# Kernel optimization log

Measured on AMD Instinct MI355X. Metric: run time of the kernel, lower is better.

The kernel has to match this reference:

```python
import jax, jax.numpy as jnp
import numpy as np

B, S, D, O, R, E = 4, 2048, 4096, 4096, 16, 8
SCALING = 32.0 / 16.0  # lora_alpha / lora_rank


def setup_inputs() -> dict:
    key = jax.random.key(0)
    ks = jax.random.split(key, 7)
    x = jax.random.normal(ks[0], (B, S, D), dtype=jnp.float32)
    W_base = jax.random.normal(ks[1], (O, D), dtype=jnp.float32) * 0.02
    b_base = jnp.zeros((O,), dtype=jnp.float32)
    A_w = jax.random.normal(ks[2], (R, D), dtype=jnp.float32) * 0.02     # lora_A weight
    B_w = jax.random.normal(ks[3], (O, R), dtype=jnp.float32) * 0.02     # lora_B weight
    router_w = jax.random.normal(ks[4], (E, D), dtype=jnp.float32) * 0.02  # router weight (core_router=False -> acts on x)
    cores = jax.random.normal(ks[5], (E, R, R), dtype=jnp.float32)       # expert rank x rank cores
    return {"x": x, "W_base": W_base, "b_base": b_base, "A_w": A_w,
            "B_w": B_w, "router_w": router_w, "cores": cores}


def reference(x, W_base, b_base, A_w, B_w, router_w, cores):
    # base linear: [B,S,O]
    result = jnp.einsum('bsd,od->bso', x, W_base) + b_base
    # lora down-projection (dropout=0 -> identity): [B,S,R]
    ax = jnp.einsum('bsd,rd->bsr', x, A_w)
    # router on x (core_router=False): softmax over experts -> [B,S,E]
    probs = jax.nn.softmax(jnp.einsum('bsd,ed->bse', x, router_w), axis=-1)
    # per-token weighted core applied to ax WITHOUT materializing [B,S,R,R]:
    # first ax through each expert core [B,S,E,R], then weight-reduce over experts.
    per_expert = jnp.einsum('bsr,erq->bseq', ax, cores)
    mixed = jnp.einsum('bseq,bse->bsq', per_expert, probs)  # [B,S,R]
    result = result + jnp.einsum('bsr,or->bso', mixed, B_w) * SCALING
    return result
```

## Files before the change

### kernel.cpp

```cpp
#include <hip/hip_runtime.h>
#include <stdint.h>

#define D_DIM 4096
#define O_DIM 4096
#define M_DIM 8192
#define SCALE_F 2.0f
#define BK 32
#define NKT 128

typedef __attribute__((ext_vector_type(4))) float f32x4;
typedef __attribute__((ext_vector_type(8))) __bf16 bf16x8;
typedef __attribute__((ext_vector_type(8))) unsigned short u16x8;

__device__ __forceinline__ unsigned short f32_to_bf16_bits(float f) {
    union { float f; uint32_t u; } v; v.f = f;
    return (unsigned short)((v.u + 0x7FFFu + ((v.u >> 16) & 1u)) >> 16);
}

__device__ __forceinline__ float dot4(f32x4 a, f32x4 b) {
    return fmaf(a.x, b.x, fmaf(a.y, b.y, fmaf(a.z, b.z, a.w * b.w)));
}

__device__ __forceinline__ int swz(int b) { return b ^ (((b >> 7) & 7) << 4); }

__global__ __launch_bounds__(256) void convert_bf16_kernel(const float* __restrict__ src,
                                                           unsigned short* __restrict__ dst,
                                                           int n4) {
    int stride = gridDim.x * blockDim.x;
    for (int i = blockIdx.x * blockDim.x + threadIdx.x; i < n4; i += stride) {
        f32x4 v = ((const f32x4*)src)[i];
        ushort4 o;
        o.x = f32_to_bf16_bits(v.x);
        o.y = f32_to_bf16_bits(v.y);
        o.z = f32_to_bf16_bits(v.z);
        o.w = f32_to_bf16_bits(v.w);
        ((ushort4*)dst)[i] = o;
    }
}

__global__ __launch_bounds__(256) void partial_mixed_kernel(const float* __restrict__ x,
                                                            const float* __restrict__ A_w,
                                                            const float* __restrict__ router_w,
                                                            unsigned short* __restrict__ xbf,
                                                            float* __restrict__ ypart) {
    __shared__ __align__(16) float Xc[32][132];
    __shared__ __align__(16) float Wc[24][132];

    const int tid = threadIdx.x;
    const int t0 = blockIdx.x * 32;
    const int d0 = blockIdx.y * 512;

    const int tg = tid >> 3;
    const int og = tid & 7;
    float acc0 = 0.f, acc1 = 0.f, acc2 = 0.f;

    for (int sub = 0; sub < 4; ++sub) {
        const int dbase = d0 + sub * 128;
        __syncthreads();
        #pragma unroll
        for (int i = 0; i < 4; ++i) {
            int idx = i * 256 + tid;
            int t = idx >> 5, dq = idx & 31;
            f32x4 v = *(const f32x4*)&x[(size_t)(t0 + t) * D_DIM + dbase + dq * 4];
            *(f32x4*)&Xc[t][dq * 4] = v;
            ushort4 o;
            o.x = f32_to_bf16_bits(v.x);
            o.y = f32_to_bf16_bits(v.y);
            o.z = f32_to_bf16_bits(v.z);
            o.w = f32_to_bf16_bits(v.w);
            *(ushort4*)&xbf[(size_t)(t0 + t) * D_DIM + dbase + dq * 4] = o;
        }
        #pragma unroll
        for (int i = 0; i < 3; ++i) {
            int idx = i * 256 + tid;
            int r = idx >> 5, dq = idx & 31;
            const float* src = (r < 16) ? (A_w + (size_t)r * D_DIM)
                                        : (router_w + (size_t)(r - 16) * D_DIM);
            *(f32x4*)&Wc[r][dq * 4] = *(const f32x4*)&src[dbase + dq * 4];
        }
        __syncthreads();
        #pragma unroll
        for (int dq = 0; dq < 32; ++dq) {
            f32x4 xv = *(const f32x4*)&Xc[tg][dq * 4];
            acc0 += dot4(xv, *(const f32x4*)&Wc[og * 3 + 0][dq * 4]);
            acc1 += dot4(xv, *(const f32x4*)&Wc[og * 3 + 1][dq * 4]);
            acc2 += dot4(xv, *(const f32x4*)&Wc[og * 3 + 2][dq * 4]);
        }
    }
    float* dst = ypart + (((size_t)blockIdx.y * 256 + blockIdx.x) * 32 + tg) * 24 + og * 3;
    dst[0] = acc0; dst[1] = acc1; dst[2] = acc2;
}

__global__ __launch_bounds__(128) void finalize_mixed_kernel(const float* __restrict__ ypart,
                                                             const float* __restrict__ cores,
                                                             float* __restrict__ mixbuf) {
    __shared__ __align__(16) float Cs[2048];
    const int tid = threadIdx.x;
    #pragma unroll
    for (int i = 0; i < 4; ++i) {
        int idx = i * 128 + tid;
        ((f32x4*)Cs)[idx] = ((const f32x4*)cores)[idx];
    }
    __syncthreads();

    const int tok = blockIdx.x * 128 + tid;
    const int tile = tok >> 5, t = tok & 31;

    float y[24];
    #pragma unroll
    for (int j = 0; j < 24; ++j) y[j] = 0.f;
    for (int ds = 0; ds < 8; ++ds) {
        const float* src = ypart + (((size_t)ds * 256 + tile) * 32 + t) * 24;
        #pragma unroll
        for (int j = 0; j < 24; ++j) y[j] += src[j];
    }

    float mx = y[16];
    #pragma unroll
    for (int e = 1; e < 8; ++e) mx = fmaxf(mx, y[16 + e]);
    float p[8], psum = 0.f;
    #pragma unroll
    for (int e = 0; e < 8; ++e) { p[e] = __expf(y[16 + e] - mx); psum += p[e]; }
    const float inv = 1.0f / psum;

    float outq[16];
    #pragma unroll
    for (int q = 0; q < 16; ++q) outq[q] = 0.f;
    for (int e = 0; e < 8; ++e) {
        const float pe = p[e] * inv;
        #pragma unroll
        for (int r = 0; r < 16; ++r) {
            const float ar = y[r] * pe;
            #pragma unroll
            for (int q = 0; q < 16; ++q)
                outq[q] = fmaf(ar, Cs[(e * 16 + r) * 16 + q], outq[q]);
        }
    }
    #pragma unroll
    for (int q = 0; q < 4; ++q) {
        f32x4 v = {outq[q * 4 + 0], outq[q * 4 + 1], outq[q * 4 + 2], outq[q * 4 + 3]};
        *(f32x4*)&mixbuf[(size_t)tok * 16 + q * 4] = v;
    }
}

__global__ __launch_bounds__(512, 2) void gemm_kernel(const unsigned short* __restrict__ xbf,
                                                      const unsigned short* __restrict__ wbf,
                                                      const float* __restrict__ bias,
                                                      const float* __restrict__ Bw,
                                                      const float* __restrict__ mixbuf,
                                                      float* __restrict__ out) {
    __shared__ __align__(16) unsigned short lds[4][2][256 * 32];

    const int bid = blockIdx.x;
    const int xcd = bid & 7;
    const int lid = bid >> 3;
    const int tm = (lid >> 4) * 8 + xcd;
    const int tn = lid & 15;
    const int m0 = tm * 256, n0 = tn * 256;

    const int tid = threadIdx.x;
    const int wave = tid >> 6, lane = tid & 63;
    const int wr = wave >> 2, wcn = wave & 3;

    int aoff[2], boff[2];
    #pragma unroll
    for (int u = 0; u < 2; ++u) {
        int c = u * 512 + tid;
        int g = swz(c * 16);
        int grow = g >> 6, gc8 = (g >> 4) & 3;
        aoff[u] = (m0 + grow) * D_DIM + gc8 * 8;
        boff[u] = (n0 + grow) * D_DIM + gc8 * 8;
    }

    const int tA = lane & 15, kq = lane >> 4;
    int aRd[8], bRd[4];
    #pragma unroll
    for (int mi = 0; mi < 8; ++mi)
        aRd[mi] = swz((wr * 128 + mi * 16 + tA) * 64 + kq * 16);
    #pragma unroll
    for (int ni = 0; ni < 4; ++ni)
        bRd[ni] = swz((wcn * 64 + ni * 16 + tA) * 64 + kq * 16);

    f32x4 acc[8][4];
    const f32x4 fz = {0.f, 0.f, 0.f, 0.f};
    #pragma unroll
    for (int mi = 0; mi < 8; ++mi)
        #pragma unroll
        for (int ni = 0; ni < 4; ++ni) acc[mi][ni] = fz;

#define STAGE_UNIT(sb, kt, u, isA)                                                        \
    do {                                                                                  \
        const unsigned short* gsrc =                                                      \
            (isA) ? (xbf + aoff[u] + (kt)*BK) : (wbf + boff[u] + (kt)*BK);                \
        __builtin_amdgcn_global_load_lds(                                                 \
            (const __attribute__((address_space(1))) void*)gsrc,                          \
            (__attribute__((address_space(3))) void*)(&lds[sb][(isA) ? 0 : 1]             \
                                                         [((u)*512 + wave * 64) * 8]),    \
            16, 0, 0);                                                                    \
    } while (0)

#define K_ITER(BUF, SBUF, KT, STG, VMC)                                                   \
    {                                                                                     \
        const char* Ab = (const char*)&lds[BUF][0][0];                                    \
        const char* Bb = (const char*)&lds[BUF][1][0];                                    \
        bf16x8 b0 = __builtin_bit_cast(bf16x8, *(const u16x8*)(Bb + bRd[0]));             \
        bf16x8 b1 = __builtin_bit_cast(bf16x8, *(const u16x8*)(Bb + bRd[1]));             \
        bf16x8 b2 = __builtin_bit_cast(bf16x8, *(const u16x8*)(Bb + bRd[2]));             \
        bf16x8 b3 = __builtin_bit_cast(bf16x8, *(const u16x8*)(Bb + bRd[3]));             \
        bf16x8 a0 = __builtin_bit_cast(bf16x8, *(const u16x8*)(Ab + aRd[0]));             \
        bf16x8 a1 = __builtin_bit_cast(bf16x8, *(const u16x8*)(Ab + aRd[1]));             \
        bf16x8 a2 = __builtin_bit_cast(bf16x8, *(const u16x8*)(Ab + aRd[2]));             \
        bf16x8 a3 = __builtin_bit_cast(bf16x8, *(const u16x8*)(Ab + aRd[3]));             \
        if (STG) {                                                                        \
            STAGE_UNIT(SBUF, KT, 0, 1);                                                   \
            STAGE_UNIT(SBUF, KT, 1, 1);                                                   \
        }                                                                                 \
        asm volatile("" ::: "memory");                                                    \
        __builtin_amdgcn_s_barrier();                                                     \
        asm volatile("" ::: "memory");                                                    \
        __builtin_amdgcn_s_setprio(1);                                                    \
        acc[0][0] = __builtin_amdgcn_mfma_f32_16x16x32_bf16(a0, b0, acc[0][0], 0, 0, 0);  \
        acc[0][1] = __builtin_amdgcn_mfma_f32_16x16x32_bf16(a0, b1, acc[0][1], 0, 0, 0);  \
        acc[0][2] = __builtin_amdgcn_mfma_f32_16x16x32_bf16(a0, b2, acc[0][2], 0, 0, 0);  \
        acc[0][3] = __builtin_amdgcn_mfma_f32_16x16x32_bf16(a0, b3, acc[0][3], 0, 0, 0);  \
        acc[1][0] = __builtin_amdgcn_mfma_f32_16x16x32_bf16(a1, b0, acc[1][0], 0, 0, 0);  \
        acc[1][1] = __builtin_amdgcn_mfma_f32_16x16x32_bf16(a1, b1, acc[1][1], 0, 0, 0);  \
        acc[1][2] = __builtin_amdgcn_mfma_f32_16x16x32_bf16(a1, b2, acc[1][2], 0, 0, 0);  \
        acc[1][3] = __builtin_amdgcn_mfma_f32_16x16x32_bf16(a1, b3, acc[1][3], 0, 0, 0);  \
        acc[2][0] = __builtin_amdgcn_mfma_f32_16x16x32_bf16(a2, b0, acc[2][0], 0, 0, 0);  \
        acc[2][1] = __builtin_amdgcn_mfma_f32_16x16x32_bf16(a2, b1, acc[2][1], 0, 0, 0);  \
        acc[2][2] = __builtin_amdgcn_mfma_f32_16x16x32_bf16(a2, b2, acc[2][2], 0, 0, 0);  \
        acc[2][3] = __builtin_amdgcn_mfma_f32_16x16x32_bf16(a2, b3, acc[2][3], 0, 0, 0);  \
        acc[3][0] = __builtin_amdgcn_mfma_f32_16x16x32_bf16(a3, b0, acc[3][0], 0, 0, 0);  \
        acc[3][1] = __builtin_amdgcn_mfma_f32_16x16x32_bf16(a3, b1, acc[3][1], 0, 0, 0);  \
        acc[3][2] = __builtin_amdgcn_mfma_f32_16x16x32_bf16(a3, b2, acc[3][2], 0, 0, 0);  \
        acc[3][3] = __builtin_amdgcn_mfma_f32_16x16x32_bf16(a3, b3, acc[3][3], 0, 0, 0);  \
        __builtin_amdgcn_s_setprio(0);                                                    \
        asm volatile("" ::: "memory");                                                    \
        __builtin_amdgcn_s_barrier();                                                     \
        asm volatile("" ::: "memory");                                                    \
        bf16x8 a4 = __builtin_bit_cast(bf16x8, *(const u16x8*)(Ab + aRd[4]));             \
        bf16x8 a5 = __builtin_bit_cast(bf16x8, *(const u16x8*)(Ab + aRd[5]));             \
        bf16x8 a6 = __builtin_bit_cast(bf16x8, *(const u16x8*)(Ab + aRd[6]));             \
        bf16x8 a7 = __builtin_bit_cast(bf16x8, *(const u16x8*)(Ab + aRd[7]));             \
        if (STG) {                                                                        \
            STAGE_UNIT(SBUF, KT, 0, 0);                                                   \
            STAGE_UNIT(SBUF, KT, 1, 0);                                                   \
        }                                                                                 \
        asm volatile("s_waitcnt vmcnt(" #VMC ")" ::: "memory");                           \
        __builtin_amdgcn_s_barrier();                                                     \
        asm volatile("" ::: "memory");                                                    \
        __builtin_amdgcn_s_setprio(1);                                                    \
        acc[4][0] = __builtin_amdgcn_mfma_f32_16x16x32_bf16(a4, b0, acc[4][0], 0, 0, 0);  \
        acc[4][1] = __builtin_amdgcn_mfma_f32_16x16x32_bf16(a4, b1, acc[4][1], 0, 0, 0);  \
        acc[4][2] = __builtin_amdgcn_mfma_f32_16x16x32_bf16(a4, b2, acc[4][2], 0, 0, 0);  \
        acc[4][3] = __builtin_amdgcn_mfma_f32_16x16x32_bf16(a4, b3, acc[4][3], 0, 0, 0);  \
        acc[5][0] = __builtin_amdgcn_mfma_f32_16x16x32_bf16(a5, b0, acc[5][0], 0, 0, 0);  \
        acc[5][1] = __builtin_amdgcn_mfma_f32_16x16x32_bf16(a5, b1, acc[5][1], 0, 0, 0);  \
        acc[5][2] = __builtin_amdgcn_mfma_f32_16x16x32_bf16(a5, b2, acc[5][2], 0, 0, 0);  \
        acc[5][3] = __builtin_amdgcn_mfma_f32_16x16x32_bf16(a5, b3, acc[5][3], 0, 0, 0);  \
        acc[6][0] = __builtin_amdgcn_mfma_f32_16x16x32_bf16(a6, b0, acc[6][0], 0, 0, 0);  \
        acc[6][1] = __builtin_amdgcn_mfma_f32_16x16x32_bf16(a6, b1, acc[6][1], 0, 0, 0);  \
        acc[6][2] = __builtin_amdgcn_mfma_f32_16x16x32_bf16(a6, b2, acc[6][2], 0, 0, 0);  \
        acc[6][3] = __builtin_amdgcn_mfma_f32_16x16x32_bf16(a6, b3, acc[6][3], 0, 0, 0);  \
        acc[7][0] = __builtin_amdgcn_mfma_f32_16x16x32_bf16(a7, b0, acc[7][0], 0, 0, 0);  \
        acc[7][1] = __builtin_amdgcn_mfma_f32_16x16x32_bf16(a7, b1, acc[7][1], 0, 0, 0);  \
        acc[7][2] = __builtin_amdgcn_mfma_f32_16x16x32_bf16(a7, b2, acc[7][2], 0, 0, 0);  \
        acc[7][3] = __builtin_amdgcn_mfma_f32_16x16x32_bf16(a7, b3, acc[7][3], 0, 0, 0);  \
        __builtin_amdgcn_s_setprio(0);                                                    \
        asm volatile("s_waitcnt lgkmcnt(0)" ::: "memory");                                \
        __builtin_amdgcn_s_barrier();                                                     \
        asm volatile("" ::: "memory");                                                    \
    }

    #pragma unroll
    for (int kt = 0; kt < 3; ++kt) {
        STAGE_UNIT(kt, kt, 0, 1);
        STAGE_UNIT(kt, kt, 1, 1);
        STAGE_UNIT(kt, kt, 0, 0);
        STAGE_UNIT(kt, kt, 1, 0);
    }
    asm volatile("s_waitcnt vmcnt(8)" ::: "memory");
    __builtin_amdgcn_s_barrier();
    asm volatile("" ::: "memory");

    for (int jj = 0; jj < 31; ++jj) {
        #pragma unroll
        for (int i = 0; i < 4; ++i) {
            const int j = jj * 4 + i;
            const int kt = j + 3;
            K_ITER(i, (i + 3) & 3, kt, 1, 8);
        }
    }
    K_ITER(0, 3, 127, 1, 8);
    K_ITER(1, 0, 0, 0, 4);
    K_ITER(2, 0, 0, 0, 0);
    K_ITER(3, 0, 0, 0, 0);
#undef K_ITER
#undef STAGE_UNIT

    const int colq = lane & 15, rq = lane >> 4;
    f32x4 bwv[4][4];
    float bcol[4];
    #pragma unroll
    for (int ni = 0; ni < 4; ++ni) {
        const int col = n0 + wcn * 64 + ni * 16 + colq;
        bcol[ni] = bias[col];
        #pragma unroll
        for (int k = 0; k < 4; ++k) bwv[ni][k] = *(const f32x4*)&Bw[(size_t)col * 16 + k * 4];
    }
    #pragma unroll
    for (int mi = 0; mi < 8; ++mi) {
        #pragma unroll
        for (int j = 0; j < 4; ++j) {
            const int row = m0 + wr * 128 + mi * 16 + rq * 4 + j;
            const f32x4* mx = (const f32x4*)&mixbuf[(size_t)row * 16];
            const f32x4 m0v = mx[0], m1v = mx[1], m2v = mx[2], m3v = mx[3];
            #pragma unroll
            for (int ni = 0; ni < 4; ++ni) {
                const int col = n0 + wcn * 64 + ni * 16 + colq;
                const float lora = dot4(m0v, bwv[ni][0]) + dot4(m1v, bwv[ni][1]) +
                                   dot4(m2v, bwv[ni][2]) + dot4(m3v, bwv[ni][3]);
                out[(size_t)row * O_DIM + col] = acc[mi][ni][j] + bcol[ni] + SCALE_F * lora;
            }
        }
    }
}

extern "C" void kernel_launch(void* const* d_in, const int* in_sizes, int n_in,
                              void* d_out, int out_size, void* d_ws, size_t ws_size,
                              hipStream_t stream) {
    const float* x        = (const float*)d_in[0];
    const float* W_base   = (const float*)d_in[1];
    const float* b_base   = (const float*)d_in[2];
    const float* A_w      = (const float*)d_in[3];
    const float* B_w      = (const float*)d_in[4];
    const float* router_w = (const float*)d_in[5];
    const float* cores    = (const float*)d_in[6];
    float* out = (float*)d_out;

    char* ws = (char*)d_ws;
    unsigned short* xbf = (unsigned short*)ws;
    unsigned short* wbf = (unsigned short*)(ws + (size_t)M_DIM * D_DIM * 2);
    char* after_w = ws + (size_t)M_DIM * D_DIM * 2 + (size_t)O_DIM * D_DIM * 2;
    float* mixbuf = (float*)after_w;
    float* ypart  = (float*)(after_w + (size_t)M_DIM * 16 * 4);

    convert_bf16_kernel<<<2048, 256, 0, stream>>>(W_base, wbf, (O_DIM * D_DIM) / 4);
    partial_mixed_kernel<<<dim3(256, 8), 256, 0, stream>>>(x, A_w, router_w, xbf, ypart);
    finalize_mixed_kernel<<<64, 128, 0, stream>>>(ypart, cores, mixbuf);
    gemm_kernel<<<512, 512, 0, stream>>>(xbf, wbf, b_base, B_w, mixbuf, out);
}
```

Measured before the change: 337.8 us.

## Fold LoRA up-projection into GEMM as extra MFMA K-step; prefetch partial loads

The scaled mixed LoRA vector and B_w are stored as bf16, zero-padded to K=32, and run through one extra MFMA K-iteration in the main GEMM. This replaces the per-output scalar dot-product epilogue, which read fp32 mixbuf and Bw for every element. The LoRA path now runs in bf16 instead of fp32, which slightly reduces its precision. The partial_mixed kernel also register-prefetches the next x and weight chunk to overlap global loads with compute, and a small kernel converts B_w to bf16.

```diff
diff --git a/kernel.cpp b/kernel.cpp
--- a/kernel.cpp
+++ b/kernel.cpp
@@ -4,7 +4,6 @@
 #define D_DIM 4096
 #define O_DIM 4096
 #define M_DIM 8192
-#define SCALE_F 2.0f
 #define BK 32
 #define NKT 128
 
@@ -38,6 +37,25 @@
     }
 }
 
+__global__ __launch_bounds__(256) void bwbf_kernel(const float* __restrict__ Bw,
+                                                   unsigned short* __restrict__ bwbf) {
+    const int o = blockIdx.x * 256 + threadIdx.x;
+    ushort4* dst = (ushort4*)&bwbf[(size_t)o * 32];
+    #pragma unroll
+    for (int g = 0; g < 4; ++g) {
+        f32x4 v = *(const f32x4*)&Bw[(size_t)o * 16 + g * 4];
+        ushort4 u;
+        u.x = f32_to_bf16_bits(v.x);
+        u.y = f32_to_bf16_bits(v.y);
+        u.z = f32_to_bf16_bits(v.z);
+        u.w = f32_to_bf16_bits(v.w);
+        dst[g] = u;
+    }
+    const ushort4 z = {0, 0, 0, 0};
+    #pragma unroll
+    for (int g = 4; g < 8; ++g) dst[g] = z;
+}
+
 __global__ __launch_bounds__(256) void partial_mixed_kernel(const float* __restrict__ x,
                                                             const float* __restrict__ A_w,
                                                             const float* __restrict__ router_w,
@@ -54,29 +72,53 @@
     const int og = tid & 7;
     float acc0 = 0.f, acc1 = 0.f, acc2 = 0.f;
 
+    int xt[4], xdq[4];
+    #pragma unroll
+    for (int i = 0; i < 4; ++i) {
+        int idx = i * 256 + tid;
+        xt[i] = idx >> 5;
+        xdq[i] = idx & 31;
+    }
+    int wrr[3], wdq[3];
+    const float* wsrc[3];
+    #pragma unroll
+    for (int i = 0; i < 3; ++i) {
+        int idx = i * 256 + tid;
+        wrr[i] = idx >> 5;
+        wdq[i] = idx & 31;
+        wsrc[i] = (wrr[i] < 16) ? (A_w + (size_t)wrr[i] * D_DIM)
+                                : (router_w + (size_t)(wrr[i] - 16) * D_DIM);
+    }
+
+    f32x4 xr[4], wreg[3];
+    #pragma unroll
+    for (int i = 0; i < 4; ++i)
+        xr[i] = *(const f32x4*)&x[(size_t)(t0 + xt[i]) * D_DIM + d0 + xdq[i] * 4];
+    #pragma unroll
+    for (int i = 0; i < 3; ++i) wreg[i] = *(const f32x4*)&wsrc[i][d0 + wdq[i] * 4];
+
     for (int sub = 0; sub < 4; ++sub) {
         const int dbase = d0 + sub * 128;
         __syncthreads();
         #pragma unroll
         for (int i = 0; i < 4; ++i) {
-            int idx = i * 256 + tid;
-            int t = idx >> 5, dq = idx & 31;
-            f32x4 v = *(const f32x4*)&x[(size_t)(t0 + t) * D_DIM + dbase + dq * 4];
-            *(f32x4*)&Xc[t][dq * 4] = v;
+            *(f32x4*)&Xc[xt[i]][xdq[i] * 4] = xr[i];
             ushort4 o;
-            o.x = f32_to_bf16_bits(v.x);
-            o.y = f32_to_bf16_bits(v.y);
-            o.z = f32_to_bf16_bits(v.z);
-            o.w = f32_to_bf16_bits(v.w);
-            *(ushort4*)&xbf[(size_t)(t0 + t) * D_DIM + dbase + dq * 4] = o;
-        }
-        #pragma unroll
-        for (int i = 0; i < 3; ++i) {
-            int idx = i * 256 + tid;
-            int r = idx >> 5, dq = idx & 31;
-            const float* src = (r < 16) ? (A_w + (size_t)r * D_DIM)
-                                        : (router_w + (size_t)(r - 16) * D_DIM);
-            *(f32x4*)&Wc[r][dq * 4] = *(const f32x4*)&src[dbase + dq * 4];
+            o.x = f32_to_bf16_bits(xr[i].x);
+            o.y = f32_to_bf16_bits(xr[i].y);
+            o.z = f32_to_bf16_bits(xr[i].z);
+            o.w = f32_to_bf16_bits(xr[i].w);
+            *(ushort4*)&xbf[(size_t)(t0 + xt[i]) * D_DIM + dbase + xdq[i] * 4] = o;
+        }
+        #pragma unroll
+        for (int i = 0; i < 3; ++i) *(f32x4*)&Wc[wrr[i]][wdq[i] * 4] = wreg[i];
+        if (sub < 3) {
+            const int nb = dbase + 128;
+            #pragma unroll
+            for (int i = 0; i < 4; ++i)
+                xr[i] = *(const f32x4*)&x[(size_t)(t0 + xt[i]) * D_DIM + nb + xdq[i] * 4];
+            #pragma unroll
+            for (int i = 0; i < 3; ++i) wreg[i] = *(const f32x4*)&wsrc[i][nb + wdq[i] * 4];
         }
         __syncthreads();
         #pragma unroll
@@ -93,7 +135,7 @@
 
 __global__ __launch_bounds__(128) void finalize_mixed_kernel(const float* __restrict__ ypart,
                                                              const float* __restrict__ cores,
-                                                             float* __restrict__ mixbuf) {
+                                                             unsigned short* __restrict__ mixbf) {
     __shared__ __align__(16) float Cs[2048];
     const int tid = threadIdx.x;
     #pragma unroll
@@ -136,18 +178,26 @@
                 outq[q] = fmaf(ar, Cs[(e * 16 + r) * 16 + q], outq[q]);
         }
     }
-    #pragma unroll
-    for (int q = 0; q < 4; ++q) {
-        f32x4 v = {outq[q * 4 + 0], outq[q * 4 + 1], outq[q * 4 + 2], outq[q * 4 + 3]};
-        *(f32x4*)&mixbuf[(size_t)tok * 16 + q * 4] = v;
-    }
+    ushort4* dst = (ushort4*)&mixbf[(size_t)tok * 32];
+    #pragma unroll
+    for (int g = 0; g < 4; ++g) {
+        ushort4 u;
+        u.x = f32_to_bf16_bits(2.0f * outq[g * 4 + 0]);
+        u.y = f32_to_bf16_bits(2.0f * outq[g * 4 + 1]);
+        u.z = f32_to_bf16_bits(2.0f * outq[g * 4 + 2]);
+        u.w = f32_to_bf16_bits(2.0f * outq[g * 4 + 3]);
+        dst[g] = u;
+    }
+    const ushort4 z = {0, 0, 0, 0};
+    #pragma unroll
+    for (int g = 4; g < 8; ++g) dst[g] = z;
 }
 
 __global__ __launch_bounds__(512, 2) void gemm_kernel(const unsigned short* __restrict__ xbf,
                                                       const unsigned short* __restrict__ wbf,
                                                       const float* __restrict__ bias,
-                                                      const float* __restrict__ Bw,
-                                                      const float* __restrict__ mixbuf,
+                                                      const unsigned short* __restrict__ mixbf,
+                                                      const unsigned short* __restrict__ bwbf,
                                                       float* __restrict__ out) {
     __shared__ __align__(16) unsigned short lds[4][2][256 * 32];
 
@@ -162,7 +212,7 @@
     const int wave = tid >> 6, lane = tid & 63;
     const int wr = wave >> 2, wcn = wave & 3;
 
-    int aoff[2], boff[2];
+    int aoff[2], boff[2], mmoff[2], mboff[2];
     #pragma unroll
     for (int u = 0; u < 2; ++u) {
         int c = u * 512 + tid;
@@ -170,6 +220,8 @@
         int grow = g >> 6, gc8 = (g >> 4) & 3;
         aoff[u] = (m0 + grow) * D_DIM + gc8 * 8;
         boff[u] = (n0 + grow) * D_DIM + gc8 * 8;
+        mmoff[u] = (m0 + grow) * 32 + gc8 * 8;
+        mboff[u] = (n0 + grow) * 32 + gc8 * 8;
     }
 
     const int tA = lane & 15, kq = lane >> 4;
@@ -195,6 +247,16 @@
         __builtin_amdgcn_global_load_lds(                                                 \
             (const __attribute__((address_space(1))) void*)gsrc,                          \
             (__attribute__((address_space(3))) void*)(&lds[sb][(isA) ? 0 : 1]             \
+                                                         [((u)*512 + wave * 64) * 8]),    \
+            16, 0, 0);                                                                    \
+    } while (0)
+
+#define STAGE_MIX(u, isA)                                                                 \
+    do {                                                                                  \
+        const unsigned short* gsrc = (isA) ? (mixbf + mmoff[u]) : (bwbf + mboff[u]);      \
+        __builtin_amdgcn_global_load_lds(                                                 \
+            (const __attribute__((address_space(1))) void*)gsrc,                          \
+            (__attribute__((address_space(3))) void*)(&lds[0][(isA) ? 0 : 1]              \
                                                          [((u)*512 + wave * 64) * 8]),    \
             16, 0, 0);                                                                    \
     } while (0)
@@ -296,32 +358,32 @@
     K_ITER(1, 0, 0, 0, 4);
     K_ITER(2, 0, 0, 0, 0);
     K_ITER(3, 0, 0, 0, 0);
+
+    STAGE_MIX(0, 1);
+    STAGE_MIX(1, 1);
+    STAGE_MIX(0, 0);
+    STAGE_MIX(1, 0);
+    asm volatile("s_waitcnt vmcnt(0)" ::: "memory");
+    __builtin_amdgcn_s_barrier();
+    asm volatile("" ::: "memory");
+    K_ITER(0, 0, 0, 0, 0);
 #undef K_ITER
+#undef STAGE_MIX
 #undef STAGE_UNIT
 
     const int colq = lane & 15, rq = lane >> 4;
-    f32x4 bwv[4][4];
     float bcol[4];
     #pragma unroll
-    for (int ni = 0; ni < 4; ++ni) {
-        const int col = n0 + wcn * 64 + ni * 16 + colq;
-        bcol[ni] = bias[col];
-        #pragma unroll
-        for (int k = 0; k < 4; ++k) bwv[ni][k] = *(const f32x4*)&Bw[(size_t)col * 16 + k * 4];
-    }
+    for (int ni = 0; ni < 4; ++ni) bcol[ni] = bias[n0 + wcn * 64 + ni * 16 + colq];
     #pragma unroll
     for (int mi = 0; mi < 8; ++mi) {
         #pragma unroll
         for (int j = 0; j < 4; ++j) {
             const int row = m0 + wr * 128 + mi * 16 + rq * 4 + j;
-            const f32x4* mx = (const f32x4*)&mixbuf[(size_t)row * 16];
-            const f32x4 m0v = mx[0], m1v = mx[1], m2v = mx[2], m3v = mx[3];
             #pragma unroll
             for (int ni = 0; ni < 4; ++ni) {
                 const int col = n0 + wcn * 64 + ni * 16 + colq;
-                const float lora = dot4(m0v, bwv[ni][0]) + dot4(m1v, bwv[ni][1]) +
-                                   dot4(m2v, bwv[ni][2]) + dot4(m3v, bwv[ni][3]);
-                out[(size_t)row * O_DIM + col] = acc[mi][ni][j] + bcol[ni] + SCALE_F * lora;
+                out[(size_t)row * O_DIM + col] = acc[mi][ni][j] + bcol[ni];
             }
         }
     }
@@ -342,12 +404,14 @@
     char* ws = (char*)d_ws;
     unsigned short* xbf = (unsigned short*)ws;
     unsigned short* wbf = (unsigned short*)(ws + (size_t)M_DIM * D_DIM * 2);
-    char* after_w = ws + (size_t)M_DIM * D_DIM * 2 + (size_t)O_DIM * D_DIM * 2;
-    float* mixbuf = (float*)after_w;
-    float* ypart  = (float*)(after_w + (size_t)M_DIM * 16 * 4);
+    char* p = ws + (size_t)M_DIM * D_DIM * 2 + (size_t)O_DIM * D_DIM * 2;
+    unsigned short* mixbf = (unsigned short*)p;
+    unsigned short* bwbf  = (unsigned short*)(p + (size_t)M_DIM * 32 * 2);
+    float* ypart = (float*)(p + (size_t)M_DIM * 32 * 2 + (size_t)O_DIM * 32 * 2);
 
     convert_bf16_kernel<<<2048, 256, 0, stream>>>(W_base, wbf, (O_DIM * D_DIM) / 4);
+    bwbf_kernel<<<O_DIM / 256, 256, 0, stream>>>(B_w, bwbf);
     partial_mixed_kernel<<<dim3(256, 8), 256, 0, stream>>>(x, A_w, router_w, xbf, ypart);
-    finalize_mixed_kernel<<<64, 128, 0, stream>>>(ypart, cores, mixbuf);
-    gemm_kernel<<<512, 512, 0, stream>>>(xbf, wbf, b_base, B_w, mixbuf, out);
-}
+    finalize_mixed_kernel<<<64, 128, 0, stream>>>(ypart, cores, mixbf);
+    gemm_kernel<<<512, 512, 0, stream>>>(xbf, wbf, b_base, mixbf, bwbf, out);
+}
```

Measured after the change: 328.0 us. -2.9%, faster.
